# Optimization experiments

Hardware: AMD Instinct MI355X
Metric: run time of the kernel (lower is better)

Reference implementation:

```python
import jax, jax.numpy as jnp
import numpy as np
from jax import lax

BN_EPS = 1e-5


def ste_sign(x):
    # binarize to {-1,+1} with straight-through estimator (BNN semantics)
    return x + lax.stop_gradient(jnp.where(x >= 0, 1.0, -1.0).astype(x.dtype) - x)


def _block(x, w, gamma, beta, pool):
    # IRPadding(1,1): pad spatial dims with -1 (binary '0' bit in hardware)
    x = jnp.pad(x, ((0, 0), (0, 0), (1, 1), (1, 1)), constant_values=-1.0)
    # IRConv2dFIN: sign-binarized weights, binary inputs, integer-valued output
    wb = ste_sign(w)
    x = lax.conv_general_dilated(x, wb, window_strides=(1, 1), padding='VALID',
                                 dimension_numbers=('NCHW', 'OIHW', 'NCHW'))
    # IRBatchNorm2d: per-channel batch-stat normalization with affine
    mean = jnp.mean(x, axis=(0, 2, 3), keepdims=True)
    var = jnp.var(x, axis=(0, 2, 3), keepdims=True)
    x = gamma[None, :, None, None] * (x - mean) * lax.rsqrt(var + BN_EPS) + beta[None, :, None, None]
    # Hardtanh then IRCLAP (sign clip to {-1,+1})
    x = jnp.clip(x, -1.0, 1.0)
    x = ste_sign(x)
    if pool:  # MaxPool2d(2,2)
        x = lax.reduce_window(x, -jnp.inf, lax.max, (1, 1, 2, 2), (1, 1, 2, 2), 'VALID')
    return x


def setup_inputs() -> dict:
    key = jax.random.key(0)
    ks = jax.random.split(key, 16)
    B = 256
    x = jnp.where(jax.random.normal(ks[0], (B, 3, 32, 32)) >= 0, 1.0, -1.0).astype(jnp.float32)
    chans = [(128, 3), (256, 128), (256, 256), (256, 256), (128, 256), (128, 128)]
    inp = {'x': x}
    for i, (co, ci) in enumerate(chans):
        n = 3 * 3 * co
        inp[f'w{i}'] = jax.random.normal(ks[1 + i], (co, ci, 3, 3), dtype=jnp.float32) * np.sqrt(2.0 / n)
        inp[f'g{i}'] = jnp.ones((co,), dtype=jnp.float32)
        inp[f'b{i}'] = jnp.zeros((co,), dtype=jnp.float32)
    inp['fc_w'] = jax.random.normal(ks[10], (10, 128 * 4 * 4), dtype=jnp.float32) * 0.01
    inp['fc_b'] = jnp.zeros((10,), dtype=jnp.float32)
    return inp


def reference(x, w0, g0, b0, w1, g1, b1, w2, g2, b2, w3, g3, b3, w4, g4, b4, w5, g5, b5, fc_w, fc_b):
    ws = [w0, w1, w2, w3, w4, w5]
    gs = [g0, g1, g2, g3, g4, g5]
    bs = [b0, b1, b2, b3, b4, b5]
    pools = [False, True, False, True, False, True]
    h = x
    for w, g, b, p in zip(ws, gs, bs, pools):
        h = _block(h, w, g, b, p)
    # flatten (dropout is identity at inference) -> fc
    h = h.reshape(h.shape[0], -1)  # [B, 128*4*4]
    return h @ fc_w.T + fc_b
```

## Files before the change

kernel.cpp:

```cpp
#include <hip/hip_runtime.h>
#include <stdint.h>

typedef unsigned long long ull;
typedef int i32x4 __attribute__((ext_vector_type(4)));
typedef int i32x16 __attribute__((ext_vector_type(16)));
#define BB 256

static const size_t OFF_CONV  = 0;
static const size_t OFF_ACT1  = 67108864;
static const size_t OFF_ACT2  = 104988672;
static const size_t OFF_BITS4 = 126222336;
static const size_t OFF_BITS5 = 127041536;
static const size_t OFF_WBPC  = 127451136;
static const size_t OFF_WPK   = 127506432;
static const size_t OFF_S     = 128980992;
static const size_t OFF_SS    = 128987136;
static const size_t OFF_ATHR  = 128999424;
static const size_t OFF_BTHR  = 129005568;
static const size_t OFF_H     = 129011712;
static const size_t OFF_XB    = 131108864;
static const size_t WS_NEEDED = 131207680;

#define SWZA(o) ((o) ^ (((((o) >> 7) ^ ((o) >> 10)) & 7) << 4))


__global__ void zero_stats_k(int* __restrict__ S, ull* __restrict__ SS) {
  int i = blockIdx.x * blockDim.x + threadIdx.x;
  if (i < 6 * 256) { S[i] = 0; SS[i] = 0ull; }
}

__global__ void pack_w_k(const float* __restrict__ w, uint32_t* __restrict__ out,
                         int co, int ci) {
  int K32 = ci >> 5;
  int total = 9 * K32 * co;
  int idx = blockIdx.x * blockDim.x + threadIdx.x;
  if (idx >= total) return;
  int c  = idx % co;
  int tk = idx / co;
  int k  = tk % K32;
  int t  = tk / K32;
  uint32_t word = 0;
  const float* wc = w + (size_t)c * ci * 9 + t;
  for (int j = 0; j < 32; ++j)
    if (wc[(size_t)(k * 32 + j) * 9] >= 0.f) word |= (1u << j);
  out[idx] = word;
}

__global__ void pack_wmfma_k(const float* __restrict__ w, signed char* __restrict__ out,
                             int co, int ci) {
  int KT = ci >> 5;
  int total = (co >> 5) * 9 * KT * 64;
  int idx = blockIdx.x * blockDim.x + threadIdx.x;
  if (idx >= total) return;
  int l   = idx & 63;
  int ctk = idx >> 6;
  int kt  = ctk % KT; int tmp = ctk / KT;
  int t   = tmp % 9;  int ct  = tmp / 9;
  int co_ = ct * 32 + (l & 31);
  int ci0 = kt * 32 + (l >> 5) * 16;
  const float* wp = w + ((size_t)co_ * ci + ci0) * 9 + t;
  int dw[4];
#pragma unroll
  for (int jj = 0; jj < 4; ++jj) {
    uint32_t d = 0;
#pragma unroll
    for (int bb = 0; bb < 4; ++bb) {
      float f = wp[(size_t)(jj * 4 + bb) * 9];
      d |= ((f >= 0.f) ? 0x01u : 0xFFu) << (8 * bb);
    }
    dw[jj] = (int)d;
  }
  *(i32x4*)(out + (size_t)idx * 16) = *(i32x4*)&dw[0];
}

__global__ void pack_x_k(const float* __restrict__ x, uint32_t* __restrict__ xbits) {
  int idx = blockIdx.x * 256 + threadIdx.x;
  if (idx >= 24576) return;
  const float* xp = x + (size_t)idx * 32;
  uint32_t w = 0;
#pragma unroll
  for (int j = 0; j < 32; ++j) if (xp[j] >= 0.f) w |= (1u << j);
  xbits[idx] = w;
}

__global__ void pack_w0_k(const float* __restrict__ w0, uint32_t* __restrict__ w27) {
  int co = threadIdx.x;
  uint32_t w = 0;
#pragma unroll
  for (int t = 0; t < 27; ++t) if (w0[co * 27 + t] >= 0.f) w |= (1u << t);
  w27[co] = w;
}

__global__ void __launch_bounds__(256) conv0x_k(
    const uint32_t* __restrict__ xbits, const uint32_t* __restrict__ w27,
    short* __restrict__ convout, int* __restrict__ Sg, ull* __restrict__ SSg) {
  int b  = blockIdx.x >> 2;
  int rg = blockIdx.x & 3;
  __shared__ uint32_t a27s[256];
  __shared__ uint32_t wlds[128];
  __shared__ int sS[256], sSS[256];
  int tid = threadIdx.x;
  if (tid < 128) wlds[tid] = w27[tid];

  int p = rg * 256 + tid;
  int y = p >> 5, xx = p & 31;
  const uint32_t* xb = xbits + (size_t)b * 96;
  uint32_t a27 = 0;
#pragma unroll
  for (int c = 0; c < 3; ++c)
#pragma unroll
    for (int kh = 0; kh < 3; ++kh) {
      int iy = y + kh - 1;
      uint32_t r = (iy >= 0 && iy < 32) ? xb[c * 32 + iy] : 0u;
      uint32_t bits3 = (uint32_t)((((uint64_t)r) << 1) >> xx) & 7u;
      a27 |= bits3 << (c * 9 + kh * 3);
    }
  a27s[tid] = a27;
  __syncthreads();

  int co = tid & 127, half = tid >> 7;
  uint32_t wv = wlds[co];
  int S = 0, SS = 0;
  int base = rg * 256 + half * 128;
  short* cb = convout + ((size_t)b * 1024 + base) * 128 + co;
  for (int i = 0; i < 128; ++i) {
    uint32_t a = a27s[half * 128 + i];
    int v = 27 - 2 * __popc(a ^ wv);
    S += v; SS += v * v;
    cb[(size_t)i * 128] = (short)v;
  }
  sS[tid] = S; sSS[tid] = SS;
  __syncthreads();
  if (tid < 128) {
    atomicAdd(&Sg[tid], sS[tid] + sS[tid + 128]);
    atomicAdd(&SSg[tid], (ull)(long long)(sSS[tid] + sSS[tid + 128]));
  }
}

__global__ void finalize_k(const int* __restrict__ S, const ull* __restrict__ SS,
                           int* __restrict__ A, int* __restrict__ B,
                           const float* __restrict__ gamma, const float* __restrict__ beta,
                           int co, int N) {
  int c = threadIdx.x;
  if (c >= co) return;
  double m  = (double)S[c] / (double)N;
  double e2 = (double)SS[c] / (double)N;
  double inv = 1.0 / sqrt(e2 - m * m + 1e-5);
  float gg = gamma[c], bb = beta[c];
  int Ai, Bi;
  if (gg > 0.f) {
    double t = m - (double)bb / ((double)gg * inv);
    t = fmin(fmax(t, -1e6), 1e6);
    Ai = 1;  Bi = (int)ceil(t);
  } else if (gg < 0.f) {
    double t = m - (double)bb / ((double)gg * inv);
    t = fmin(fmax(t, -1e6), 1e6);
    Ai = -1; Bi = -(int)floor(t);
  } else {
    Ai = 0;  Bi = (bb >= 0.f) ? 0 : 1;
  }
  A[c] = Ai; B[c] = Bi;
}

__global__ void binarize_k(const short* __restrict__ conv, int co, int H, int W, int pool,
                           uint32_t* __restrict__ out_bits, signed char* __restrict__ out8,
                           const int* __restrict__ A, const int* __restrict__ B,
                           float* __restrict__ hout) {
  __shared__ int As[256], Bs[256];
  int tid = threadIdx.x;
  for (int i = tid; i < co; i += 256) { As[i] = A[i]; Bs[i] = B[i]; }
  __syncthreads();

  int K32 = co >> 5;
  int Ho = pool ? (H >> 1) : H, Wo = pool ? (W >> 1) : W;
  int PH = Ho + 2, PW = Wo + 2;
  int total = BB * K32 * PH * PW;
  int idx = blockIdx.x * 256 + tid;
  if (idx >= total) return;
  int k  = idx % K32;
  int t1 = idx / K32;
  int px = t1 % PW; int t2 = t1 / PW;
  int py = t2 % PH; int b  = t2 / PH;
  uint32_t word = 0;
  if (py >= 1 && py <= Ho && px >= 1 && px <= Wo) {
    int oy = py - 1, ox = px - 1;
    int np = pool ? 2 : 1;
    for (int dy = 0; dy < np; ++dy)
      for (int dx = 0; dx < np; ++dx) {
        int iy = oy * np + dy, ix = ox * np + dx;
        const short* cp = conv + ((size_t)((b * H + iy) * W + ix)) * co + k * 32;
#pragma unroll
        for (int j = 0; j < 32; ++j) {
          int v = cp[j];
          int c = k * 32 + j;
          if (As[c] * v >= Bs[c]) word |= (1u << j);
        }
      }
    if (hout) {
#pragma unroll
      for (int j = 0; j < 32; ++j) {
        int c = k * 32 + j;
        hout[((size_t)(b * 128 + c) * 4 + oy) * 4 + ox] = ((word >> j) & 1) ? 1.f : -1.f;
      }
    }
  }
  if (out_bits)
    out_bits[((size_t)(b * K32 + k) * PH + py) * PW + px] = word;
  if (out8) {
    int dw[8];
#pragma unroll
    for (int jj = 0; jj < 8; ++jj) {
      uint32_t d = 0;
#pragma unroll
      for (int bb = 0; bb < 4; ++bb)
        d |= (((word >> (jj * 4 + bb)) & 1) ? 0x01u : 0xFFu) << (8 * bb);
      dw[jj] = (int)d;
    }
    signed char* p = out8 + (((size_t)(b * PH + py)) * PW + px) * (size_t)co + k * 32;
    *(i32x4*)p = *(i32x4*)&dw[0];
    *(i32x4*)(p + 16) = *(i32x4*)&dw[4];
  }
}

template <int CI, int W, int CO_BLK>
__global__ __launch_bounds__(256, 2) void conv_mfma_k(
    const signed char* __restrict__ act, const i32x4* __restrict__ wpk,
    short* __restrict__ convout, int* __restrict__ Sg, ull* __restrict__ SSg) {
  constexpr int KT = CI / 32;
  constexpr int PW = W + 2;
  constexpr int TR = 32 / W;
  constexpr int ROWS_BLK = 4 * TR;
  constexpr int NBY = W / ROWS_BLK;
  constexpr int AROWS = ROWS_BLK + 2;
  constexpr int ABYTES = AROWS * PW * CI;
  constexpr int NSTEP = 9 * KT;
  constexpr int NT = CO_BLK / 64;

  __shared__ __attribute__((aligned(16))) char ldsA[ABYTES];

  int tid = threadIdx.x;
  int b = blockIdx.x / NBY, blk_y = blockIdx.x % NBY;
  int y0 = blk_y * ROWS_BLK;

  const signed char* src = act + ((size_t)b * (W + 2) + y0) * PW * CI;
  for (int o = tid * 16; o < ABYTES; o += 4096) {
    i32x4 v = *(const i32x4*)(src + o);
    *(i32x4*)(ldsA + SWZA(o)) = v;
  }
  __syncthreads();

  int l = tid & 63, w = tid >> 6;
  int wm = w & 1, wn = w >> 1;
  int r = l & 31, khalf = l >> 5;
  int px = (TR == 1) ? r : (r & 15);

  int inv[2];
#pragma unroll
  for (int m = 0; m < 2; ++m) {
    int ti = wm * 2 + m;
    int row = (TR == 1) ? ti : (ti * 2 + (r >> 4));
    inv[m] = (row * PW + px) * CI + khalf * 16;
  }
  const i32x4* wl = wpk + l;

  i32x16 acc[2][NT];
#pragma unroll
  for (int m = 0; m < 2; ++m)
#pragma unroll
    for (int n = 0; n < NT; ++n)
#pragma unroll
      for (int q = 0; q < 16; ++q) acc[m][n][q] = 0;

  auto LOADS = [&](int s, i32x4 (&a)[2], i32x4 (&bf)[NT]) {
    int t = s / KT, kt = s % KT;
    int soff = ((t / 3) * PW + (t % 3)) * CI + kt * 32;
#pragma unroll
    for (int m = 0; m < 2; ++m) {
      int o = inv[m] + soff;
      o = SWZA(o);
      a[m] = *(const i32x4*)(ldsA + o);
    }
#pragma unroll
    for (int n = 0; n < NT; ++n)
      bf[n] = wl[(size_t)(((wn * NT + n) * 9 + t) * KT + kt) * 64];
  };
  auto MFMAALL = [&](i32x4 (&a)[2], i32x4 (&bf)[NT]) {
#pragma unroll
    for (int m = 0; m < 2; ++m)
#pragma unroll
      for (int n = 0; n < NT; ++n)
        acc[m][n] = __builtin_amdgcn_mfma_i32_32x32x32_i8(a[m], bf[n], acc[m][n], 0, 0, 0);
  };

  i32x4 aA[2], bA[NT], aB[2], bB[NT];
  LOADS(0, aA, bA);
  int s = 0;
  for (; s + 2 < NSTEP; s += 2) {
    LOADS(s + 1, aB, bB);
    MFMAALL(aA, bA);
    LOADS(s + 2, aA, bA);
    MFMAALL(aB, bB);
  }
  LOADS(NSTEP - 1, aB, bB);
  MFMAALL(aA, bA);
  MFMAALL(aB, bB);

#pragma unroll
  for (int n = 0; n < NT; ++n) {
    int s1 = 0, s2 = 0;
#pragma unroll
    for (int m = 0; m < 2; ++m) {
      int ti = wm * 2 + m;
      i32x16 v = acc[m][n];
      int pk[8];
#pragma unroll
      for (int q = 0; q < 8; ++q) {
        int v0 = v[2 * q], v1 = v[2 * q + 1];
        s1 += v0 + v1; s2 += v0 * v0 + v1 * v1;
        pk[q] = (v0 & 0xffff) | (v1 << 16);
      }
      int fragLocal = ti * (2 * NT) + wn * NT + n;
      size_t baseS = (((size_t)blockIdx.x * (8 * NT) + fragLocal) * 64 + l) * 16;
      *(i32x4*)(convout + baseS) = *(i32x4*)&pk[0];
      *(i32x4*)(convout + baseS + 8) = *(i32x4*)&pk[4];
    }
    s1 += __shfl_xor(s1, 32);
    s2 += __shfl_xor(s2, 32);
    if (l < 32) {
      int ch = wn * (NT * 32) + n * 32 + l;
      atomicAdd(&Sg[ch], s1);
      atomicAdd(&SSg[ch], (ull)(long long)s2);
    }
  }
}

template <int CO_BLK, int W, int POOL, int OUT_BITS, int OUTP>
__global__ __launch_bounds__(256) void binarize_frag_k(
    const short* __restrict__ convout, signed char* __restrict__ out8,
    uint32_t* __restrict__ out_bits, const int* __restrict__ Ath,
    const int* __restrict__ Bth, int co_base) {
  constexpr int TR = 32 / W;
  constexpr int ROWS_BLK = 4 * TR;
  constexpr int NBY = W / ROWS_BLK;
  constexpr int K32B = CO_BLK / 32;
  constexpr int NT = CO_BLK / 64;
  constexpr int Wout = POOL ? W / 2 : W;
  constexpr int HoutB = POOL ? ROWS_BLK / 2 : ROWS_BLK;
  constexpr int WORDS = HoutB * Wout * K32B;
  constexpr int NP = POOL ? 2 : 1;
  constexpr int LBYTES = 128 * CO_BLK * 2;

  __shared__ __attribute__((aligned(16))) char ldsC[LBYTES];
  int tid = threadIdx.x;
  int b = blockIdx.x / NBY, blk_y = blockIdx.x % NBY;

  const char* src = (const char*)(convout + (size_t)blockIdx.x * (128 * CO_BLK));
  for (int o = tid * 16; o < LBYTES; o += 4096) {
    i32x4 v = *(const i32x4*)(src + o);
    int so = o ^ (((o >> 11) & 7) << 4);
    *(i32x4*)(ldsC + so) = v;
  }
  __syncthreads();

  for (int widx = tid; widx < WORDS; widx += 256) {
    int k = widx % K32B, opx = widx / K32B;
    int oy = opx / Wout, ox = opx % Wout;
    int wn = k / NT, n = k % NT;
    int bases[NP * NP];
#pragma unroll
    for (int dy = 0; dy < NP; ++dy)
#pragma unroll
      for (int dx = 0; dx < NP; ++dx) {
        int yl = POOL ? oy * 2 + dy : oy;
        int x  = POOL ? ox * 2 + dx : ox;
        int ti = yl / TR;
        int rr = (TR == 1) ? x : ((yl & 1) * 16 + x);
        int hi = (rr >> 2) & 1, q = (rr & 3) + 4 * (rr >> 3);
        int fragLocal = ti * K32B + wn * NT + n;
        bases[dy * NP + dx] = ((fragLocal * 64 + hi * 32) * 16 + q) * 2;
      }
    uint32_t word = 0;
    for (int j = 0; j < 32; ++j) {
      int c = k * 32 + j;
      int Aj = Ath[c], Bj = Bth[c];
      int mx = -0x7fffffff;
#pragma unroll
      for (int p2 = 0; p2 < NP * NP; ++p2) {
        int bo = bases[p2] + j * 32;
        bo ^= ((bo >> 11) & 7) << 4;
        int v = *(const short*)(ldsC + bo);
        int av = Aj * v;
        mx = (av > mx) ? av : mx;
      }
      if (mx >= Bj) word |= (1u << j);
    }
    int gy = blk_y * HoutB + oy, gx = ox;
    if (OUT_BITS) {
      out_bits[(((size_t)b * K32B + k) * OUTP + 1 + gy) * OUTP + 1 + gx] = word;
    } else {
      size_t a0 = (((size_t)b * OUTP + (1 + gy)) * OUTP + (1 + gx)) * 256 + co_base + k * 32;
      int dw[8];
#pragma unroll
      for (int jj = 0; jj < 8; ++jj) {
        uint32_t d = 0;
#pragma unroll
        for (int bb = 0; bb < 4; ++bb)
          d |= (((word >> (jj * 4 + bb)) & 1) ? 0x01u : 0xFFu) << (8 * bb);
        dw[jj] = (int)d;
      }
      *(i32x4*)(out8 + a0) = *(i32x4*)&dw[0];
      *(i32x4*)(out8 + a0 + 16) = *(i32x4*)&dw[4];
    }
  }
}

template <int K32>
__global__ void __launch_bounds__(256) conv_xnor_k(
    const uint32_t* __restrict__ act, const uint32_t* __restrict__ wb,
    short* __restrict__ convout, int* __restrict__ Sg, ull* __restrict__ SSg,
    int co, int H, int Ktot) {
  int Hp  = H + 2;
  int T   = H >> 3;
  int cot = co >> 6;
  int TT  = T * T * cot;
  int b   = blockIdx.x / TT;
  int r   = blockIdx.x % TT;
  int ct  = r % cot;
  int tt  = r / cot;
  int ty  = tt / T, tx = tt % T;
  int co_base = ct << 6;

  __shared__ __attribute__((aligned(16))) uint32_t ldsA[K32 * 10 * 12];
  __shared__ __attribute__((aligned(16))) uint32_t ldsB[9 * K32 * 64];
  __shared__ int sS[64];
  __shared__ int sSS[64];

  int tid = threadIdx.x;
  if (tid < 64) { sS[tid] = 0; sSS[tid] = 0; }
  for (int i = tid; i < 9 * K32 * 64; i += 256) {
    int c  = i & 63;
    int tk = i >> 6;
    ldsB[i] = wb[(size_t)tk * co + co_base + c];
  }
  const uint32_t* ab = act + (size_t)b * K32 * Hp * Hp;
  for (int i = tid; i < K32 * 100; i += 256) {
    int k  = i / 100;
    int rr = i % 100;
    int yy = rr / 10, xx = rr % 10;
    ldsA[(k * 10 + yy) * 12 + xx] = ab[(size_t)(k * Hp + ty * 8 + yy) * Hp + tx * 8 + xx];
  }
  __syncthreads();

  int tc   = tid & 15;
  int pgp  = tid >> 4;
  int yrow = pgp >> 1;
  int xg   = pgp & 1;

  int acc[4][4];
#pragma unroll
  for (int i = 0; i < 4; ++i)
#pragma unroll
    for (int j = 0; j < 4; ++j) acc[i][j] = 0;

#pragma unroll 1
  for (int k = 0; k < K32; ++k) {
#pragma unroll
    for (int kh = 0; kh < 3; ++kh) {
      int abase = (k * 10 + yrow + kh) * 12 + xg * 4;
      uint4 a0 = *(const uint4*)&ldsA[abase];
      uint2 a1 = *(const uint2*)&ldsA[abase + 4];
      uint32_t arow[6] = {a0.x, a0.y, a0.z, a0.w, a1.x, a1.y};
#pragma unroll
      for (int kw = 0; kw < 3; ++kw) {
        int t = kh * 3 + kw;
        uint4 bwv = *(const uint4*)&ldsB[(t * K32 + k) * 64 + tc * 4];
        uint32_t bwa[4] = {bwv.x, bwv.y, bwv.z, bwv.w};
#pragma unroll
        for (int pi = 0; pi < 4; ++pi) {
          uint32_t aw = arow[pi + kw];
#pragma unroll
          for (int cj = 0; cj < 4; ++cj)
            acc[pi][cj] += __popc(aw ^ bwa[cj]);
        }
      }
    }
  }

  int vS[4] = {0, 0, 0, 0}, vSS[4] = {0, 0, 0, 0};
  int gy0 = ty * 8 + yrow, gx0 = tx * 8 + xg * 4;
#pragma unroll
  for (int pi = 0; pi < 4; ++pi) {
    short4 vv;
    int v0 = Ktot - 2 * acc[pi][0];
    int v1 = Ktot - 2 * acc[pi][1];
    int v2 = Ktot - 2 * acc[pi][2];
    int v3 = Ktot - 2 * acc[pi][3];
    vS[0] += v0; vSS[0] += v0 * v0;
    vS[1] += v1; vSS[1] += v1 * v1;
    vS[2] += v2; vSS[2] += v2 * v2;
    vS[3] += v3; vSS[3] += v3 * v3;
    vv.x = (short)v0; vv.y = (short)v1; vv.z = (short)v2; vv.w = (short)v3;
    size_t obase = ((size_t)(b * H + gy0) * H + (gx0 + pi)) * co + co_base + tc * 4;
    *(short4*)&convout[obase] = vv;
  }
#pragma unroll
  for (int cj = 0; cj < 4; ++cj) {
    atomicAdd(&sS[tc * 4 + cj], vS[cj]);
    atomicAdd(&sSS[tc * 4 + cj], vSS[cj]);
  }
  __syncthreads();
  if (tid < 64) {
    atomicAdd(&Sg[co_base + tid], sS[tid]);
    atomicAdd(&SSg[co_base + tid], (ull)(long long)sSS[tid]);
  }
}

__global__ void fc_k(const float* __restrict__ h, const float* __restrict__ fcw,
                     const float* __restrict__ fcb, float* __restrict__ out) {
  int b = blockIdx.x;
  int tid = threadIdx.x;
  int j = tid & 15;
  int chunk = tid >> 4;
  __shared__ float red[16][17];
  float acc = 0.f;
  if (j < 10) {
    const float* hp = h + (size_t)b * 2048 + chunk * 128;
    const float* wp = fcw + (size_t)j * 2048 + chunk * 128;
    for (int i = 0; i < 128; ++i) acc += hp[i] * wp[i];
  }
  red[chunk][j] = acc;
  __syncthreads();
  if (tid < 10) {
    float s = fcb[tid];
    for (int c = 0; c < 16; ++c) s += red[c][tid];
    out[b * 10 + tid] = s;
  }
}


extern "C" void kernel_launch(void* const* d_in, const int* in_sizes, int n_in,
                              void* d_out, int out_size, void* d_ws, size_t ws_size,
                              hipStream_t stream) {
  (void)in_sizes; (void)n_in; (void)out_size;
  if (ws_size < WS_NEEDED) return;

  const float* x = (const float*)d_in[0];
  const float* w[6]; const float* g[6]; const float* bt[6];
  for (int i = 0; i < 6; ++i) {
    w[i]  = (const float*)d_in[1 + 3 * i];
    g[i]  = (const float*)d_in[2 + 3 * i];
    bt[i] = (const float*)d_in[3 + 3 * i];
  }
  const float* fcw = (const float*)d_in[19];
  const float* fcb = (const float*)d_in[20];

  char* ws = (char*)d_ws;
  short*        convout = (short*)(ws + OFF_CONV);
  signed char*  act1    = (signed char*)(ws + OFF_ACT1);
  signed char*  act2    = (signed char*)(ws + OFF_ACT2);
  uint32_t*     bits4   = (uint32_t*)(ws + OFF_BITS4);
  uint32_t*     bits5   = (uint32_t*)(ws + OFF_BITS5);
  uint32_t*     wbpc    = (uint32_t*)(ws + OFF_WBPC);
  signed char*  wpkc    = (signed char*)(ws + OFF_WPK);
  int*          Sg      = (int*)(ws + OFF_S);
  ull*          SSg     = (ull*)(ws + OFF_SS);
  int*          Athr    = (int*)(ws + OFF_ATHR);
  int*          Bthr    = (int*)(ws + OFF_BTHR);
  float*        hbuf    = (float*)(ws + OFF_H);
  uint32_t*     xbits   = (uint32_t*)(ws + OFF_XB);
  uint32_t*     w27     = xbits + 24576;
  float*        out     = (float*)d_out;

  const i32x4* wpk1 = (const i32x4*)wpkc;
  const i32x4* wpk2 = wpk1 + 294912 / 16;
  const i32x4* wpk3 = wpk1 + 884736 / 16;

  zero_stats_k<<<6, 256, 0, stream>>>(Sg, SSg);

  pack_w_k<<<36, 256, 0, stream>>>(w[4], wbpc, 128, 256);
  pack_w_k<<<18, 256, 0, stream>>>(w[5], wbpc + 9216, 128, 128);
  pack_wmfma_k<<<72, 256, 0, stream>>>(w[1], wpkc, 256, 128);
  pack_wmfma_k<<<144, 256, 0, stream>>>(w[2], wpkc + 294912, 256, 256);
  pack_wmfma_k<<<144, 256, 0, stream>>>(w[3], wpkc + 884736, 256, 256);
  pack_x_k<<<96, 256, 0, stream>>>(x, xbits);
  pack_w0_k<<<1, 128, 0, stream>>>(w[0], w27);

  hipMemsetAsync(act2, 0xFF, 21233664, stream);
  hipMemsetAsync(bits4, 0x00, 819200, stream);

  conv0x_k<<<256 * 4, 256, 0, stream>>>(xbits, w27, convout, Sg, SSg);
  finalize_k<<<1, 256, 0, stream>>>(Sg, SSg, Athr, Bthr, g[0], bt[0], 128, 262144);
  binarize_k<<<(256 * 4 * 34 * 34 + 255) / 256, 256, 0, stream>>>(
      convout, 128, 32, 32, 0, nullptr, act1, Athr, Bthr, nullptr);

  conv_mfma_k<128, 32, 128><<<2048, 256, 0, stream>>>(act1, wpk1, convout, Sg + 256, SSg + 256);
  finalize_k<<<1, 256, 0, stream>>>(Sg + 256, SSg + 256, Athr + 256, Bthr + 256, g[1], bt[1], 128, 262144);
  binarize_frag_k<128, 32, 1, 0, 18><<<2048, 256, 0, stream>>>(
      convout, act2, nullptr, Athr + 256, Bthr + 256, 0);

  conv_mfma_k<128, 32, 128><<<2048, 256, 0, stream>>>(act1, wpk1 + 9216, convout, Sg + 384, SSg + 384);
  finalize_k<<<1, 256, 0, stream>>>(Sg + 384, SSg + 384, Athr + 384, Bthr + 384, g[1] + 128, bt[1] + 128, 128, 262144);
  hipMemsetAsync(act1, 0xFF, 21233664, stream);
  binarize_frag_k<128, 32, 1, 0, 18><<<2048, 256, 0, stream>>>(
      convout, act2, nullptr, Athr + 384, Bthr + 384, 128);

  conv_mfma_k<256, 16, 256><<<512, 256, 0, stream>>>(act2, wpk2, convout, Sg + 512, SSg + 512);
  finalize_k<<<1, 256, 0, stream>>>(Sg + 512, SSg + 512, Athr + 512, Bthr + 512, g[2], bt[2], 256, 65536);
  binarize_frag_k<256, 16, 0, 0, 18><<<512, 256, 0, stream>>>(
      convout, act1, nullptr, Athr + 512, Bthr + 512, 0);

  conv_mfma_k<256, 16, 256><<<512, 256, 0, stream>>>(act1, wpk3, convout, Sg + 768, SSg + 768);
  finalize_k<<<1, 256, 0, stream>>>(Sg + 768, SSg + 768, Athr + 768, Bthr + 768, g[3], bt[3], 256, 65536);
  binarize_frag_k<256, 16, 1, 1, 10><<<512, 256, 0, stream>>>(
      convout, nullptr, bits4, Athr + 768, Bthr + 768, 0);

  conv_xnor_k<8><<<256 * 2, 256, 0, stream>>>(bits4, wbpc, convout,
                                              Sg + 1024, SSg + 1024, 128, 8, 2304);
  finalize_k<<<1, 256, 0, stream>>>(Sg + 1024, SSg + 1024, Athr + 1024, Bthr + 1024, g[4], bt[4], 128, 16384);
  binarize_k<<<(256 * 4 * 10 * 10 + 255) / 256, 256, 0, stream>>>(
      convout, 128, 8, 8, 0, bits5, nullptr, Athr + 1024, Bthr + 1024, nullptr);

  conv_xnor_k<4><<<256 * 2, 256, 0, stream>>>(bits5, wbpc + 9216, convout,
                                              Sg + 1280, SSg + 1280, 128, 8, 1152);
  finalize_k<<<1, 256, 0, stream>>>(Sg + 1280, SSg + 1280, Athr + 1280, Bthr + 1280, g[5], bt[5], 128, 16384);
  binarize_k<<<(256 * 4 * 6 * 6 + 255) / 256, 256, 0, stream>>>(
      convout, 128, 8, 8, 1, bits4, nullptr, Athr + 1280, Bthr + 1280, hbuf);

  fc_k<<<256, 256, 0, stream>>>(hbuf, fcw, fcb, out);
}
```

Before: 648.3 us.

## Fix MFMA conv to 128-channel blocks and prefetch weights in 4-step chunks

The MFMA conv kernel now always computes 128 output channels per launch, so the 256-channel layers 2 and 3 are split into two half-channel conv/finalize/binarize passes. The inner loop is restructured to prefetch weight fragments for four K-steps at a time into double buffers, while LDS activation reads are issued just before their MFMAs. binarize_frag gains a total-word-count parameter so bit outputs land at the right channel offset. The aim is fewer accumulator registers (better occupancy) and deeper latency hiding on weight loads, at the cost of reloading activations twice and more launches.

After: 652.4 us. No clear change (+0.6%).

```diff
diff --git a/kernel.cpp b/kernel.cpp
--- a/kernel.cpp
+++ b/kernel.cpp
@@ -222,7 +222,7 @@
   }
 }
 
-template <int CI, int W, int CO_BLK>
+template <int CI, int W>
 __global__ __launch_bounds__(256, 2) void conv_mfma_k(
     const signed char* __restrict__ act, const i32x4* __restrict__ wpk,
     short* __restrict__ convout, int* __restrict__ Sg, ull* __restrict__ SSg) {
@@ -234,7 +234,7 @@
   constexpr int AROWS = ROWS_BLK + 2;
   constexpr int ABYTES = AROWS * PW * CI;
   constexpr int NSTEP = 9 * KT;
-  constexpr int NT = CO_BLK / 64;
+  constexpr int NC = NSTEP / 4;
 
   __shared__ __attribute__((aligned(16))) char ldsA[ABYTES];
 
@@ -263,50 +263,52 @@
   }
   const i32x4* wl = wpk + l;
 
-  i32x16 acc[2][NT];
+  i32x16 acc[2][2];
 #pragma unroll
   for (int m = 0; m < 2; ++m)
 #pragma unroll
-    for (int n = 0; n < NT; ++n)
+    for (int n = 0; n < 2; ++n)
 #pragma unroll
       for (int q = 0; q < 16; ++q) acc[m][n][q] = 0;
 
-  auto LOADS = [&](int s, i32x4 (&a)[2], i32x4 (&bf)[NT]) {
-    int t = s / KT, kt = s % KT;
-    int soff = ((t / 3) * PW + (t % 3)) * CI + kt * 32;
-#pragma unroll
-    for (int m = 0; m < 2; ++m) {
-      int o = inv[m] + soff;
-      o = SWZA(o);
-      a[m] = *(const i32x4*)(ldsA + o);
-    }
-#pragma unroll
-    for (int n = 0; n < NT; ++n)
-      bf[n] = wl[(size_t)(((wn * NT + n) * 9 + t) * KT + kt) * 64];
-  };
-  auto MFMAALL = [&](i32x4 (&a)[2], i32x4 (&bf)[NT]) {
-#pragma unroll
-    for (int m = 0; m < 2; ++m)
-#pragma unroll
-      for (int n = 0; n < NT; ++n)
-        acc[m][n] = __builtin_amdgcn_mfma_i32_32x32x32_i8(a[m], bf[n], acc[m][n], 0, 0, 0);
-  };
-
-  i32x4 aA[2], bA[NT], aB[2], bB[NT];
-  LOADS(0, aA, bA);
-  int s = 0;
-  for (; s + 2 < NSTEP; s += 2) {
-    LOADS(s + 1, aB, bB);
-    MFMAALL(aA, bA);
-    LOADS(s + 2, aA, bA);
-    MFMAALL(aB, bB);
-  }
-  LOADS(NSTEP - 1, aB, bB);
-  MFMAALL(aA, bA);
-  MFMAALL(aB, bB);
-
-#pragma unroll
-  for (int n = 0; n < NT; ++n) {
+  i32x4 bA[2][4], bB[2][4];
+
+#define PB(buf, c)                                                             \
+  if ((c) < NC) {                                                              \
+    _Pragma("unroll") for (int ph = 0; ph < 4; ++ph) {                         \
+      int s = (c) * 4 + ph; int t = s / KT, kt = s % KT;                       \
+      _Pragma("unroll") for (int n = 0; n < 2; ++n)                            \
+        buf[n][ph] = wl[(size_t)(((wn * 2 + n) * 9 + t) * KT + kt) * 64];      \
+    }                                                                          \
+  }
+
+#define DC(buf, c)                                                             \
+  {                                                                            \
+    _Pragma("unroll") for (int ph = 0; ph < 4; ++ph) {                         \
+      int s = (c) * 4 + ph; int t = s / KT, kt = s % KT;                       \
+      int soff = ((t / 3) * PW + (t % 3)) * CI + kt * 32;                      \
+      i32x4 a0, a1;                                                            \
+      { int o = SWZA(inv[0] + soff); a0 = *(const i32x4*)(ldsA + o); }         \
+      { int o = SWZA(inv[1] + soff); a1 = *(const i32x4*)(ldsA + o); }         \
+      _Pragma("unroll") for (int n = 0; n < 2; ++n) {                          \
+        acc[0][n] = __builtin_amdgcn_mfma_i32_32x32x32_i8(a0, buf[n][ph], acc[0][n], 0, 0, 0); \
+        acc[1][n] = __builtin_amdgcn_mfma_i32_32x32x32_i8(a1, buf[n][ph], acc[1][n], 0, 0, 0); \
+      }                                                                        \
+    }                                                                          \
+  }
+
+  PB(bA, 0);
+  for (int c = 0; c < NC; c += 2) {
+    PB(bB, c + 1);
+    DC(bA, c);
+    PB(bA, c + 2);
+    if (c + 1 < NC) DC(bB, c + 1);
+  }
+#undef PB
+#undef DC
+
+#pragma unroll
+  for (int n = 0; n < 2; ++n) {
     int s1 = 0, s2 = 0;
 #pragma unroll
     for (int m = 0; m < 2; ++m) {
@@ -319,22 +321,22 @@
         s1 += v0 + v1; s2 += v0 * v0 + v1 * v1;
         pk[q] = (v0 & 0xffff) | (v1 << 16);
       }
-      int fragLocal = ti * (2 * NT) + wn * NT + n;
-      size_t baseS = (((size_t)blockIdx.x * (8 * NT) + fragLocal) * 64 + l) * 16;
+      int fragLocal = ti * 4 + wn * 2 + n;
+      size_t baseS = (((size_t)blockIdx.x * 16 + fragLocal) * 64 + l) * 16;
       *(i32x4*)(convout + baseS) = *(i32x4*)&pk[0];
       *(i32x4*)(convout + baseS + 8) = *(i32x4*)&pk[4];
     }
     s1 += __shfl_xor(s1, 32);
     s2 += __shfl_xor(s2, 32);
     if (l < 32) {
-      int ch = wn * (NT * 32) + n * 32 + l;
+      int ch = wn * 64 + n * 32 + l;
       atomicAdd(&Sg[ch], s1);
       atomicAdd(&SSg[ch], (ull)(long long)s2);
     }
   }
 }
 
-template <int CO_BLK, int W, int POOL, int OUT_BITS, int OUTP>
+template <int CO_BLK, int W, int POOL, int OUT_BITS, int OUTP, int K32TOT>
 __global__ __launch_bounds__(256) void binarize_frag_k(
     const short* __restrict__ convout, signed char* __restrict__ out8,
     uint32_t* __restrict__ out_bits, const int* __restrict__ Ath,
@@ -396,7 +398,7 @@
     }
     int gy = blk_y * HoutB + oy, gx = ox;
     if (OUT_BITS) {
-      out_bits[(((size_t)b * K32B + k) * OUTP + 1 + gy) * OUTP + 1 + gx] = word;
+      out_bits[(((size_t)b * K32TOT + (co_base >> 5) + k) * OUTP + 1 + gy) * OUTP + 1 + gx] = word;
     } else {
       size_t a0 = (((size_t)b * OUTP + (1 + gy)) * OUTP + (1 + gx)) * 256 + co_base + k * 32;
       int dw[8];
@@ -593,26 +595,36 @@
   binarize_k<<<(256 * 4 * 34 * 34 + 255) / 256, 256, 0, stream>>>(
       convout, 128, 32, 32, 0, nullptr, act1, Athr, Bthr, nullptr);
 
-  conv_mfma_k<128, 32, 128><<<2048, 256, 0, stream>>>(act1, wpk1, convout, Sg + 256, SSg + 256);
+  conv_mfma_k<128, 32><<<2048, 256, 0, stream>>>(act1, wpk1, convout, Sg + 256, SSg + 256);
   finalize_k<<<1, 256, 0, stream>>>(Sg + 256, SSg + 256, Athr + 256, Bthr + 256, g[1], bt[1], 128, 262144);
-  binarize_frag_k<128, 32, 1, 0, 18><<<2048, 256, 0, stream>>>(
+  binarize_frag_k<128, 32, 1, 0, 18, 8><<<2048, 256, 0, stream>>>(
       convout, act2, nullptr, Athr + 256, Bthr + 256, 0);
 
-  conv_mfma_k<128, 32, 128><<<2048, 256, 0, stream>>>(act1, wpk1 + 9216, convout, Sg + 384, SSg + 384);
+  conv_mfma_k<128, 32><<<2048, 256, 0, stream>>>(act1, wpk1 + 9216, convout, Sg + 384, SSg + 384);
   finalize_k<<<1, 256, 0, stream>>>(Sg + 384, SSg + 384, Athr + 384, Bthr + 384, g[1] + 128, bt[1] + 128, 128, 262144);
   hipMemsetAsync(act1, 0xFF, 21233664, stream);
-  binarize_frag_k<128, 32, 1, 0, 18><<<2048, 256, 0, stream>>>(
+  binarize_frag_k<128, 32, 1, 0, 18, 8><<<2048, 256, 0, stream>>>(
       convout, act2, nullptr, Athr + 384, Bthr + 384, 128);
 
-  conv_mfma_k<256, 16, 256><<<512, 256, 0, stream>>>(act2, wpk2, convout, Sg + 512, SSg + 512);
-  finalize_k<<<1, 256, 0, stream>>>(Sg + 512, SSg + 512, Athr + 512, Bthr + 512, g[2], bt[2], 256, 65536);
-  binarize_frag_k<256, 16, 0, 0, 18><<<512, 256, 0, stream>>>(
+  conv_mfma_k<256, 16><<<512, 256, 0, stream>>>(act2, wpk2, convout, Sg + 512, SSg + 512);
+  finalize_k<<<1, 256, 0, stream>>>(Sg + 512, SSg + 512, Athr + 512, Bthr + 512, g[2], bt[2], 128, 65536);
+  binarize_frag_k<128, 16, 0, 0, 18, 8><<<512, 256, 0, stream>>>(
       convout, act1, nullptr, Athr + 512, Bthr + 512, 0);
 
-  conv_mfma_k<256, 16, 256><<<512, 256, 0, stream>>>(act1, wpk3, convout, Sg + 768, SSg + 768);
-  finalize_k<<<1, 256, 0, stream>>>(Sg + 768, SSg + 768, Athr + 768, Bthr + 768, g[3], bt[3], 256, 65536);
-  binarize_frag_k<256, 16, 1, 1, 10><<<512, 256, 0, stream>>>(
+  conv_mfma_k<256, 16><<<512, 256, 0, stream>>>(act2, wpk2 + 18432, convout, Sg + 640, SSg + 640);
+  finalize_k<<<1, 256, 0, stream>>>(Sg + 640, SSg + 640, Athr + 640, Bthr + 640, g[2] + 128, bt[2] + 128, 128, 65536);
+  binarize_frag_k<128, 16, 0, 0, 18, 8><<<512, 256, 0, stream>>>(
+      convout, act1, nullptr, Athr + 640, Bthr + 640, 128);
+
+  conv_mfma_k<256, 16><<<512, 256, 0, stream>>>(act1, wpk3, convout, Sg + 768, SSg + 768);
+  finalize_k<<<1, 256, 0, stream>>>(Sg + 768, SSg + 768, Athr + 768, Bthr + 768, g[3], bt[3], 128, 65536);
+  binarize_frag_k<128, 16, 1, 1, 10, 8><<<512, 256, 0, stream>>>(
       convout, nullptr, bits4, Athr + 768, Bthr + 768, 0);
+
+  conv_mfma_k<256, 16><<<512, 256, 0, stream>>>(act1, wpk3 + 18432, convout, Sg + 896, SSg + 896);
+  finalize_k<<<1, 256, 0, stream>>>(Sg + 896, SSg + 896, Athr + 896, Bthr + 896, g[3] + 128, bt[3] + 128, 128, 65536);
+  binarize_frag_k<128, 16, 1, 1, 10, 8><<<512, 256, 0, stream>>>(
+      convout, nullptr, bits4, Athr + 896, Bthr + 896, 128);
 
   conv_xnor_k<8><<<256 * 2, 256, 0, stream>>>(bits4, wbpc, convout,
                                               Sg + 1024, SSg + 1024, 128, 8, 2304);
```
